# Kernel optimization log

Measured on AMD Instinct MI355X. Metric: run time of the kernel, lower is better.

## Reference

```python
import jax, jax.numpy as jnp
import numpy as np

EPS = 1e-8


def _laplace_normalize(edge_row, edge_col, edge_vals, num_nodes):
    # D_r^{-1/2} A D_c^{-1/2} as in laplace_transform
    deg_r = jax.ops.segment_sum(edge_vals, edge_row, num_segments=num_nodes)
    deg_c = jax.ops.segment_sum(edge_vals, edge_col, num_segments=num_nodes)
    inv_r = 1.0 / (jnp.sqrt(deg_r) + EPS)
    inv_c = 1.0 / (jnp.sqrt(deg_c) + EPS)
    return edge_vals * inv_r[edge_row] * inv_c[edge_col]


def _l2norm(x):
    # F.normalize(p=2, dim=1): x / max(||x||, eps) with eps=1e-12
    n = jnp.sqrt(jnp.sum(x * x, axis=1, keepdims=True))
    return x / jnp.maximum(n, 1e-12)


def setup_inputs() -> dict:
    key = jax.random.key(0)
    k1, k2, k3, k4, k5, k6 = jax.random.split(key, 6)
    N, D, E, B = 100000, 64, 3200000, 4096
    node_features = jax.random.normal(k1, (N, D), dtype=jnp.float32)
    edge_row = jax.random.randint(k2, (E,), 0, N, dtype=jnp.int32)
    edge_col = jax.random.randint(k3, (E,), 0, N, dtype=jnp.int32)
    edge_vals = jnp.ones((E,), dtype=jnp.float32)
    a_id = jax.random.randint(k4, (B,), 0, N, dtype=jnp.int32)
    pos_id = jax.random.randint(k5, (B,), 0, N, dtype=jnp.int32)
    neg_id = jax.random.randint(k6, (B,), 0, N, dtype=jnp.int32)
    return {"node_features": node_features, "edge_row": edge_row,
            "edge_col": edge_col, "edge_vals": edge_vals,
            "a_id": a_id, "pos_id": pos_id, "neg_id": neg_id}


def reference(node_features, edge_row, edge_col, edge_vals, a_id, pos_id, neg_id):
    num_nodes = node_features.shape[0]
    num_layers = 3
    norm_vals = _laplace_normalize(edge_row, edge_col, edge_vals, num_nodes)

    # one_propagate: repeated spmm + per-layer L2 normalize, mean over layers
    features = node_features
    acc = node_features  # layer-0 term of the running sum (not normalized)
    for _ in range(num_layers):
        msgs = norm_vals[:, None] * features[edge_col]  # [E, D]
        features = jax.ops.segment_sum(msgs, edge_row, num_segments=num_nodes)
        acc = acc + _l2norm(features)
    node_rep = acc / (num_layers + 1)

    # BPR loss over batch
    a = node_rep[a_id]
    pos_pred = jnp.sum(a * node_rep[pos_id], axis=1)
    neg_pred = jnp.sum(a * node_rep[neg_id], axis=1)
    loss = jnp.mean(-jax.nn.log_sigmoid(pos_pred - neg_pred))
    return loss
```

## Files before the change

kernel.cpp:

```cpp
#include <hip/hip_runtime.h>
#include <math.h>

#define DDIM 64
#define BUCKET 1024
#define LRSHIFT 17
#define CMASK 0x1FFFF
#define LRMASK 0x3FF
#define NBLK 512
#define TPB_BIN 1024
#define NWV 16
#define MAXNB 128

typedef unsigned long long ull;
typedef _Float16 half2_t __attribute__((ext_vector_type(2)));

__device__ inline unsigned int bf16_hi(float v) {
    unsigned int a = __float_as_uint(v);
    return (a + 0x7fffu + ((a >> 16) & 1u)) & 0xffff0000u;
}

__device__ inline unsigned int pk_f16x2(float lo, float hi) {
    return __builtin_bit_cast(unsigned int, __builtin_amdgcn_cvt_pkrtz(lo, hi));
}

__device__ inline half2_t dup_lo16(unsigned int s) {
    return __builtin_bit_cast(half2_t, __builtin_amdgcn_perm(0u, s, 0x01000100u));
}

__device__ inline half2_t h2_shfl_xor(half2_t v, int off) {
    return __builtin_bit_cast(half2_t, __shfl_xor(__builtin_bit_cast(unsigned int, v), off));
}

__global__ void init_fill_kernel(int* __restrict__ gfill_r, int* __restrict__ gfill_c,
                                 int NB, int cap) {
    int k = blockIdx.x * blockDim.x + threadIdx.x;
    if (k < NB) {
        gfill_r[k * 16] = k * cap;
        gfill_c[k * 16] = k * cap;
    }
}

__global__ __launch_bounds__(TPB_BIN)
void binning_kernel(const int* __restrict__ erow, const int* __restrict__ ecol,
                    const float* __restrict__ evals,
                    int* __restrict__ gfill_r, int* __restrict__ gfill_c,
                    ull* __restrict__ br, unsigned int* __restrict__ bc,
                    int E, int NB, int chunk) {
    __shared__ int hr[NWV][MAXNB];
    __shared__ int hc[NWV][MAXNB];
    __shared__ int fr[MAXNB];
    __shared__ int fc[MAXNB];
    int t = threadIdx.x;
    int wv = t >> 6;
    for (int k = t; k < NWV * MAXNB; k += TPB_BIN) { (&hr[0][0])[k] = 0; (&hc[0][0])[k] = 0; }
    __syncthreads();
    int lo = blockIdx.x * chunk;
    int hi = min(E, lo + chunk);
    int nq = (hi - lo) >> 2;
    int rem = (hi - lo) & 3;
    int p0 = t, p1 = t + TPB_BIN;
    bool h0 = p0 < nq, h1 = p1 < nq;
    int4 r40, c40, r41, c41;
    float4 v40, v41;
    if (h0) {
        int i = lo + 4 * p0;
        r40 = *(const int4*)(erow + i);
        c40 = *(const int4*)(ecol + i);
        v40 = *(const float4*)(evals + i);
        atomicAdd(&hr[wv][r40.x >> 10], 1);
        atomicAdd(&hr[wv][r40.y >> 10], 1);
        atomicAdd(&hr[wv][r40.z >> 10], 1);
        atomicAdd(&hr[wv][r40.w >> 10], 1);
        atomicAdd(&hc[wv][c40.x >> 10], 1);
        atomicAdd(&hc[wv][c40.y >> 10], 1);
        atomicAdd(&hc[wv][c40.z >> 10], 1);
        atomicAdd(&hc[wv][c40.w >> 10], 1);
    }
    if (h1) {
        int i = lo + 4 * p1;
        r41 = *(const int4*)(erow + i);
        c41 = *(const int4*)(ecol + i);
        v41 = *(const float4*)(evals + i);
        atomicAdd(&hr[wv][r41.x >> 10], 1);
        atomicAdd(&hr[wv][r41.y >> 10], 1);
        atomicAdd(&hr[wv][r41.z >> 10], 1);
        atomicAdd(&hr[wv][r41.w >> 10], 1);
        atomicAdd(&hc[wv][c41.x >> 10], 1);
        atomicAdd(&hc[wv][c41.y >> 10], 1);
        atomicAdd(&hc[wv][c41.z >> 10], 1);
        atomicAdd(&hc[wv][c41.w >> 10], 1);
    }
    if (t == 0) {
        for (int i = hi - rem; i < hi; i++) {
            atomicAdd(&hr[0][erow[i] >> 10], 1);
            atomicAdd(&hc[0][ecol[i] >> 10], 1);
        }
    }
    __syncthreads();
    if (t < NB) {
        int sr = 0, sc = 0;
        #pragma unroll
        for (int w2 = 0; w2 < NWV; w2++) { sr += hr[w2][t]; sc += hc[w2][t]; }
        fr[t] = atomicAdd(&gfill_r[t * 16], sr);
        fc[t] = atomicAdd(&gfill_c[t * 16], sc);
    }
    __syncthreads();
    if (h0) {
        int pos0 = atomicAdd(&fr[r40.x >> 10], 1);
        int pos1 = atomicAdd(&fr[r40.y >> 10], 1);
        int pos2 = atomicAdd(&fr[r40.z >> 10], 1);
        int pos3 = atomicAdd(&fr[r40.w >> 10], 1);
        br[pos0] = ((ull)__float_as_uint(v40.x) << 32) | ((ull)(r40.x & 1023) << LRSHIFT) | (unsigned)c40.x;
        br[pos1] = ((ull)__float_as_uint(v40.y) << 32) | ((ull)(r40.y & 1023) << LRSHIFT) | (unsigned)c40.y;
        br[pos2] = ((ull)__float_as_uint(v40.z) << 32) | ((ull)(r40.z & 1023) << LRSHIFT) | (unsigned)c40.z;
        br[pos3] = ((ull)__float_as_uint(v40.w) << 32) | ((ull)(r40.w & 1023) << LRSHIFT) | (unsigned)c40.w;
        int q0 = atomicAdd(&fc[c40.x >> 10], 1);
        int q1 = atomicAdd(&fc[c40.y >> 10], 1);
        int q2 = atomicAdd(&fc[c40.z >> 10], 1);
        int q3 = atomicAdd(&fc[c40.w >> 10], 1);
        bc[q0] = bf16_hi(v40.x) | (unsigned)(c40.x & 1023);
        bc[q1] = bf16_hi(v40.y) | (unsigned)(c40.y & 1023);
        bc[q2] = bf16_hi(v40.z) | (unsigned)(c40.z & 1023);
        bc[q3] = bf16_hi(v40.w) | (unsigned)(c40.w & 1023);
    }
    if (h1) {
        int pos0 = atomicAdd(&fr[r41.x >> 10], 1);
        int pos1 = atomicAdd(&fr[r41.y >> 10], 1);
        int pos2 = atomicAdd(&fr[r41.z >> 10], 1);
        int pos3 = atomicAdd(&fr[r41.w >> 10], 1);
        br[pos0] = ((ull)__float_as_uint(v41.x) << 32) | ((ull)(r41.x & 1023) << LRSHIFT) | (unsigned)c41.x;
        br[pos1] = ((ull)__float_as_uint(v41.y) << 32) | ((ull)(r41.y & 1023) << LRSHIFT) | (unsigned)c41.y;
        br[pos2] = ((ull)__float_as_uint(v41.z) << 32) | ((ull)(r41.z & 1023) << LRSHIFT) | (unsigned)c41.z;
        br[pos3] = ((ull)__float_as_uint(v41.w) << 32) | ((ull)(r41.w & 1023) << LRSHIFT) | (unsigned)c41.w;
        int q0 = atomicAdd(&fc[c41.x >> 10], 1);
        int q1 = atomicAdd(&fc[c41.y >> 10], 1);
        int q2 = atomicAdd(&fc[c41.z >> 10], 1);
        int q3 = atomicAdd(&fc[c41.w >> 10], 1);
        bc[q0] = bf16_hi(v41.x) | (unsigned)(c41.x & 1023);
        bc[q1] = bf16_hi(v41.y) | (unsigned)(c41.y & 1023);
        bc[q2] = bf16_hi(v41.z) | (unsigned)(c41.z & 1023);
        bc[q3] = bf16_hi(v41.w) | (unsigned)(c41.w & 1023);
    }
    if (t == 0) {
        for (int i = hi - rem; i < hi; i++) {
            int r = erow[i], c = ecol[i];
            float v = evals[i];
            int pos = atomicAdd(&fr[r >> 10], 1);
            br[pos] = ((ull)__float_as_uint(v) << 32) | ((ull)(r & 1023) << LRSHIFT) | (unsigned)c;
            int pos2 = atomicAdd(&fc[c >> 10], 1);
            bc[pos2] = bf16_hi(v) | (unsigned)(c & 1023);
        }
    }
}

__global__ __launch_bounds__(BUCKET)
void fused_cp_kernel(const ull* __restrict__ br, const unsigned int* __restrict__ bc,
                     const int* __restrict__ gfill_r, const int* __restrict__ gfill_c,
                     int2* __restrict__ rse, float* __restrict__ inv_c,
                     unsigned int* __restrict__ cw, int N, int cap) {
    __shared__ int   cnt[BUCKET];
    __shared__ float ds[BUCKET];
    __shared__ float dsc[BUCKET];
    __shared__ int   sc[BUCKET];
    __shared__ float invr[BUCKET];
    int b = blockIdx.x, t = threadIdx.x;
    cnt[t] = 0; ds[t] = 0.0f; dsc[t] = 0.0f;
    __syncthreads();
    int s = b * cap;
    int e = gfill_r[b * 16];
    int m = s + ((e - s) & ~3);
    for (int i = s + 4 * t; i < m; i += 4 * BUCKET) {
        ull p0 = br[i];
        ull p1 = br[i + 1];
        ull p2 = br[i + 2];
        ull p3 = br[i + 3];
        int lr0 = (int)((p0 >> LRSHIFT) & LRMASK);
        int lr1 = (int)((p1 >> LRSHIFT) & LRMASK);
        int lr2 = (int)((p2 >> LRSHIFT) & LRMASK);
        int lr3 = (int)((p3 >> LRSHIFT) & LRMASK);
        atomicAdd(&cnt[lr0], 1);
        atomicAdd(&cnt[lr1], 1);
        atomicAdd(&cnt[lr2], 1);
        atomicAdd(&cnt[lr3], 1);
        atomicAdd(&ds[lr0], __uint_as_float((unsigned)(p0 >> 32)));
        atomicAdd(&ds[lr1], __uint_as_float((unsigned)(p1 >> 32)));
        atomicAdd(&ds[lr2], __uint_as_float((unsigned)(p2 >> 32)));
        atomicAdd(&ds[lr3], __uint_as_float((unsigned)(p3 >> 32)));
    }
    if (t == 0) {
        for (int i = m; i < e; i++) {
            ull p = br[i];
            int lr = (int)((p >> LRSHIFT) & LRMASK);
            atomicAdd(&cnt[lr], 1);
            atomicAdd(&ds[lr], __uint_as_float((unsigned)(p >> 32)));
        }
    }
    int e2 = gfill_c[b * 16];
    int m2 = s + ((e2 - s) & ~3);
    for (int i = s + 4 * t; i < m2; i += 4 * BUCKET) {
        uint4 p = *(const uint4*)(bc + i);
        atomicAdd(&dsc[p.x & 0x3FFu], __uint_as_float(p.x & 0xffff0000u));
        atomicAdd(&dsc[p.y & 0x3FFu], __uint_as_float(p.y & 0xffff0000u));
        atomicAdd(&dsc[p.z & 0x3FFu], __uint_as_float(p.z & 0xffff0000u));
        atomicAdd(&dsc[p.w & 0x3FFu], __uint_as_float(p.w & 0xffff0000u));
    }
    if (t == 0) {
        for (int i = m2; i < e2; i++) {
            unsigned int p = bc[i];
            atomicAdd(&dsc[p & 0x3FFu], __uint_as_float(p & 0xffff0000u));
        }
    }
    __syncthreads();
    int c0 = cnt[t];
    int sum4 = (c0 + 3) & ~3;
    sc[t] = sum4;
    __syncthreads();
    for (int off = 1; off < BUCKET; off <<= 1) {
        int v = (t >= off) ? sc[t - off] : 0;
        __syncthreads();
        sc[t] += v;
        __syncthreads();
    }
    int st = s + sc[t] - sum4;
    int node = b * BUCKET + t;
    if (node < N) {
        int2 se;
        se.x = st;
        se.y = st + c0;
        rse[node] = se;
    }
    inv_c[node] = 1.0f / (sqrtf(dsc[t]) + 1e-8f);
    invr[t] = 1.0f / (sqrtf(ds[t]) + 1e-8f);
    __syncthreads();
    cnt[t] = st;
    __syncthreads();
    for (int i = s + 4 * t; i < m; i += 4 * BUCKET) {
        ull p0 = br[i];
        ull p1 = br[i + 1];
        ull p2 = br[i + 2];
        ull p3 = br[i + 3];
        int c0_ = (int)(p0 & CMASK), c1_ = (int)(p1 & CMASK);
        int c2_ = (int)(p2 & CMASK), c3_ = (int)(p3 & CMASK);
        int lr0 = (int)((p0 >> LRSHIFT) & LRMASK);
        int lr1 = (int)((p1 >> LRSHIFT) & LRMASK);
        int lr2 = (int)((p2 >> LRSHIFT) & LRMASK);
        int lr3 = (int)((p3 >> LRSHIFT) & LRMASK);
        float v0 = __uint_as_float((unsigned)(p0 >> 32));
        float v1 = __uint_as_float((unsigned)(p1 >> 32));
        float v2 = __uint_as_float((unsigned)(p2 >> 32));
        float v3 = __uint_as_float((unsigned)(p3 >> 32));
        int pos0 = atomicAdd(&cnt[lr0], 1);
        int pos1 = atomicAdd(&cnt[lr1], 1);
        int pos2 = atomicAdd(&cnt[lr2], 1);
        int pos3 = atomicAdd(&cnt[lr3], 1);
        float w0 = v0 * invr[lr0];
        float w1 = v1 * invr[lr1];
        float w2 = v2 * invr[lr2];
        float w3 = v3 * invr[lr3];
        cw[pos0] = ((unsigned)c0_ << 15) | ((pk_f16x2(w0, w0) & 0xFFFFu) >> 1);
        cw[pos1] = ((unsigned)c1_ << 15) | ((pk_f16x2(w1, w1) & 0xFFFFu) >> 1);
        cw[pos2] = ((unsigned)c2_ << 15) | ((pk_f16x2(w2, w2) & 0xFFFFu) >> 1);
        cw[pos3] = ((unsigned)c3_ << 15) | ((pk_f16x2(w3, w3) & 0xFFFFu) >> 1);
    }
    if (t == 0) {
        for (int i = m; i < e; i++) {
            ull p = br[i];
            int c = (int)(p & CMASK);
            int lr = (int)((p >> LRSHIFT) & LRMASK);
            float v = __uint_as_float((unsigned)(p >> 32));
            int pos = atomicAdd(&cnt[lr], 1);
            float wv = v * invr[lr];
            cw[pos] = ((unsigned)c << 15) | ((pk_f16x2(wv, wv) & 0xFFFFu) >> 1);
        }
    }
}

__global__ void cvt_kernel(const float* __restrict__ src, const float* __restrict__ inv_c,
                           unsigned int* __restrict__ dst, long n4) {
    long i = (long)blockIdx.x * blockDim.x + threadIdx.x;
    if (i < n4) {
        float ic = inv_c[i >> 4];
        float4 v = ((const float4*)src)[i];
        uint2 o;
        o.x = pk_f16x2(v.x * ic, v.y * ic);
        o.y = pk_f16x2(v.z * ic, v.w * ic);
        ((uint2*)dst)[i] = o;
    }
}

__global__ __launch_bounds__(256)
void spmm_f16_kernel(const int2* __restrict__ rse,
                     const unsigned int* __restrict__ cw,
                     const float* __restrict__ inv_c,
                     const unsigned short* __restrict__ fin,
                     unsigned short* __restrict__ fout, int N) {
    int wid = blockIdx.x * (blockDim.x >> 6) + (threadIdx.x >> 6);
    if (wid >= N) return;
    int lane = threadIdx.x & 63;
    int g = lane >> 3;
    int h = lane & 7;
    int2 se = rse[wid];
    float ic = inv_c[wid];
    int s = se.x, e = se.y;
    half2_t a2[8];
    #pragma unroll
    for (int k = 0; k < 8; k++) a2[k] = (half2_t)0;

    for (int base = s; base < e; base += 32) {
        int j = base + 4 * g;
        if (j < e) {
            uint4 pw = *(const uint4*)(cw + j);
            int c0 = (int)(pw.x >> 15);
            int c1 = (j + 1 < e) ? (int)(pw.y >> 15) : c0;
            int c2 = (j + 2 < e) ? (int)(pw.z >> 15) : c0;
            int c3 = (j + 3 < e) ? (int)(pw.w >> 15) : c0;
            uint4 q0 = ((const uint4*)(fin + ((long)c0 << 6)))[h];
            uint4 q1 = ((const uint4*)(fin + ((long)c1 << 6)))[h];
            uint4 q2 = ((const uint4*)(fin + ((long)c2 << 6)))[h];
            uint4 q3 = ((const uint4*)(fin + ((long)c3 << 6)))[h];
            half2_t w0 = dup_lo16(pw.x << 1);
            half2_t w1 = (j + 1 < e) ? dup_lo16(pw.y << 1) : (half2_t)0;
            half2_t w2 = (j + 2 < e) ? dup_lo16(pw.z << 1) : (half2_t)0;
            half2_t w3 = (j + 3 < e) ? dup_lo16(pw.w << 1) : (half2_t)0;
            a2[0] += w0 * __builtin_bit_cast(half2_t, q0.x);
            a2[1] += w0 * __builtin_bit_cast(half2_t, q0.y);
            a2[2] += w0 * __builtin_bit_cast(half2_t, q0.z);
            a2[3] += w0 * __builtin_bit_cast(half2_t, q0.w);
            a2[4] += w1 * __builtin_bit_cast(half2_t, q1.x);
            a2[5] += w1 * __builtin_bit_cast(half2_t, q1.y);
            a2[6] += w1 * __builtin_bit_cast(half2_t, q1.z);
            a2[7] += w1 * __builtin_bit_cast(half2_t, q1.w);
            a2[0] += w2 * __builtin_bit_cast(half2_t, q2.x);
            a2[1] += w2 * __builtin_bit_cast(half2_t, q2.y);
            a2[2] += w2 * __builtin_bit_cast(half2_t, q2.z);
            a2[3] += w2 * __builtin_bit_cast(half2_t, q2.w);
            a2[4] += w3 * __builtin_bit_cast(half2_t, q3.x);
            a2[5] += w3 * __builtin_bit_cast(half2_t, q3.y);
            a2[6] += w3 * __builtin_bit_cast(half2_t, q3.z);
            a2[7] += w3 * __builtin_bit_cast(half2_t, q3.w);
        }
    }

    #pragma unroll
    for (int k = 0; k < 4; k++) a2[k] += a2[k + 4];
    #pragma unroll
    for (int k = 0; k < 4; k++) {
        a2[k] += h2_shfl_xor(a2[k], 8);
        a2[k] += h2_shfl_xor(a2[k], 16);
        a2[k] += h2_shfl_xor(a2[k], 32);
    }
    if (g == 0) {
        half2_t ich = __builtin_bit_cast(half2_t, pk_f16x2(ic, ic));
        uint4 o;
        o.x = __builtin_bit_cast(unsigned int, a2[0] * ich);
        o.y = __builtin_bit_cast(unsigned int, a2[1] * ich);
        o.z = __builtin_bit_cast(unsigned int, a2[2] * ich);
        o.w = __builtin_bit_cast(unsigned int, a2[3] * ich);
        ((uint4*)(fout + ((long)wid << 6)))[h] = o;
    }
}

__device__ inline float rep_at(const float* __restrict__ nf,
                               const unsigned short* __restrict__ f1,
                               const unsigned short* __restrict__ f2,
                               const unsigned short* __restrict__ f3,
                               int id, int lane) {
    long off = (long)id * DDIM + lane;
    float r  = nf[off];
    float v1 = (float)__builtin_bit_cast(_Float16, f1[off]);
    float v2 = (float)__builtin_bit_cast(_Float16, f2[off]);
    float v3 = (float)__builtin_bit_cast(_Float16, f3[off]);
    float s1 = v1 * v1, s2 = v2 * v2, s3 = v3 * v3;
    #pragma unroll
    for (int o = 1; o < 64; o <<= 1) {
        s1 += __shfl_xor(s1, o);
        s2 += __shfl_xor(s2, o);
        s3 += __shfl_xor(s3, o);
    }
    r += v1 / fmaxf(sqrtf(s1), 1e-12f);
    r += v2 / fmaxf(sqrtf(s2), 1e-12f);
    r += v3 / fmaxf(sqrtf(s3), 1e-12f);
    return r;
}

__global__ void loss_terms_kernel(const float* __restrict__ nf,
                                  const unsigned short* __restrict__ f1,
                                  const unsigned short* __restrict__ f2,
                                  const unsigned short* __restrict__ f3,
                                  const int* __restrict__ a_id, const int* __restrict__ p_id,
                                  const int* __restrict__ n_id,
                                  float* __restrict__ terms, int B) {
    long gid = (long)blockIdx.x * blockDim.x + threadIdx.x;
    int b = (int)(gid >> 6);
    int lane = threadIdx.x & 63;
    if (b < B) {
        float ra = rep_at(nf, f1, f2, f3, a_id[b], lane);
        float rp = rep_at(nf, f1, f2, f3, p_id[b], lane);
        float rn = rep_at(nf, f1, f2, f3, n_id[b], lane);
        float dp = ra * rp, dn = ra * rn;
        #pragma unroll
        for (int off = 1; off < 64; off <<= 1) { dp += __shfl_xor(dp, off); dn += __shfl_xor(dn, off); }
        if (lane == 0) {
            float x = (dp - dn) * 0.0625f;
            terms[b] = fmaxf(-x, 0.0f) + log1pf(expf(-fabsf(x)));
        }
    }
}

__global__ void reduce_kernel(const float* __restrict__ terms, float* __restrict__ out, int B) {
    __shared__ float sm[256];
    float s = 0.0f;
    for (int i = threadIdx.x; i < B; i += 256) s += terms[i];
    sm[threadIdx.x] = s;
    __syncthreads();
    for (int stride = 128; stride > 0; stride >>= 1) {
        if (threadIdx.x < stride) sm[threadIdx.x] += sm[threadIdx.x + stride];
        __syncthreads();
    }
    if (threadIdx.x == 0) out[0] = sm[0] / (float)B;
}

extern "C" void kernel_launch(void* const* d_in, const int* in_sizes, int n_in,
                              void* d_out, int out_size, void* d_ws, size_t ws_size,
                              hipStream_t stream) {
    const float* nf    = (const float*)d_in[0];
    const int*   erow  = (const int*)d_in[1];
    const int*   ecol  = (const int*)d_in[2];
    const float* evals = (const float*)d_in[3];
    const int*   a_id  = (const int*)d_in[4];
    const int*   p_id  = (const int*)d_in[5];
    const int*   n_id  = (const int*)d_in[6];

    int N = in_sizes[0] / DDIM;
    int E = in_sizes[1];
    int B = in_sizes[4];
    int NB = (N + BUCKET - 1) / BUCKET;
    int chunk = (((E + NBLK - 1) / NBLK) + 3) & ~3;
    int Npad = NB * BUCKET;

    long capl = ((long)E * BUCKET) / N;
    int cap = (int)(capl + capl / 12 + 5120);
    cap = (cap + 63) & ~63;

    size_t regionA = (size_t)cap * NB * 8;
    size_t regionB = (size_t)cap * NB * 4;
    size_t featB16 = (size_t)N * DDIM * 2;
    if (regionA < 2 * featB16) regionA = 2 * featB16;

    char* w = (char*)d_ws;
    ull*  br     = (ull*)w;
    char* regAp  = w;                 w += regionA;
    unsigned int* bc = (unsigned int*)w;
    unsigned int* cw = (unsigned int*)w;  w += regionB + 256;
    unsigned short* fb2 = (unsigned short*)w;  w += featB16;
    float* inv_c = (float*)w;         w += (size_t)Npad * 4;
    int2* rse    = (int2*)w;          w += (size_t)N * 8;
    int* gfill_r = (int*)w;           w += (size_t)NB * 16 * 4;
    int* gfill_c = (int*)w;           w += (size_t)NB * 16 * 4;
    float* terms = (float*)w;         w += (size_t)B * 4;

    unsigned short* fb0 = (unsigned short*)regAp;
    unsigned short* fb1 = (unsigned short*)(regAp + featB16);

    init_fill_kernel<<<1, 128, 0, stream>>>(gfill_r, gfill_c, NB, cap);
    binning_kernel<<<NBLK, TPB_BIN, 0, stream>>>(erow, ecol, evals, gfill_r, gfill_c,
                                                 br, bc, E, NB, chunk);
    fused_cp_kernel<<<NB, BUCKET, 0, stream>>>(br, bc, gfill_r, gfill_c,
                                               rse, inv_c, cw, N, cap);

    long n4 = (long)N * DDIM / 4;
    cvt_kernel<<<(unsigned)((n4 + 255) / 256), 256, 0, stream>>>(nf, inv_c, (unsigned int*)fb0, n4);

    unsigned spmmGrid = (unsigned)((N + 3) / 4);
    spmm_f16_kernel<<<spmmGrid, 256, 0, stream>>>(rse, cw, inv_c, fb0, fb1, N);
    spmm_f16_kernel<<<spmmGrid, 256, 0, stream>>>(rse, cw, inv_c, fb1, fb2, N);
    spmm_f16_kernel<<<spmmGrid, 256, 0, stream>>>(rse, cw, inv_c, fb2, fb0, N);

    loss_terms_kernel<<<(unsigned)(((long)B * 64 + 255) / 256), 256, 0, stream>>>(
        nf, fb1, fb2, fb0, a_id, p_id, n_id, terms, B);
    reduce_kernel<<<1, 256, 0, stream>>>(terms, (float*)d_out, B);
}
```

Baseline: 410.8 us.

## Split fused degree/CSR build kernel into four sub-blocks per row bucket

The fused kernel that computes degrees and builds the compressed-row layout now launches four blocks per 1024-node bucket instead of one. Every block still recomputes the full bucket's row counts and prefix scan. Each block then handles only its 256-node quarter for the degree sums, the inverse norms and the scatter of packed column/weight entries. The aim is to fill more compute units, since there are only about a hundred buckets. The cost is reading each bucket's edge data four times and repeating the count and scan work.

After: 358.3 us. -12.8%, faster.

```diff
diff --git a/kernel.cpp b/kernel.cpp
--- a/kernel.cpp
+++ b/kernel.cpp
@@ -3,6 +3,7 @@
 
 #define DDIM 64
 #define BUCKET 1024
+#define SUBB 256
 #define LRSHIFT 17
 #define CMASK 0x1FFFF
 #define LRMASK 0x3FF
@@ -153,18 +154,21 @@
     }
 }
 
-__global__ __launch_bounds__(BUCKET)
+__global__ __launch_bounds__(1024)
 void fused_cp_kernel(const ull* __restrict__ br, const unsigned int* __restrict__ bc,
                      const int* __restrict__ gfill_r, const int* __restrict__ gfill_c,
                      int2* __restrict__ rse, float* __restrict__ inv_c,
                      unsigned int* __restrict__ cw, int N, int cap) {
     __shared__ int   cnt[BUCKET];
-    __shared__ float ds[BUCKET];
-    __shared__ float dsc[BUCKET];
     __shared__ int   sc[BUCKET];
-    __shared__ float invr[BUCKET];
-    int b = blockIdx.x, t = threadIdx.x;
-    cnt[t] = 0; ds[t] = 0.0f; dsc[t] = 0.0f;
+    __shared__ float ds[SUBB];
+    __shared__ float dsc[SUBB];
+    __shared__ float invr[SUBB];
+    __shared__ int   cur[SUBB];
+    int b = blockIdx.x >> 2, q = blockIdx.x & 3;
+    int t = threadIdx.x;
+    cnt[t] = 0;
+    if (t < SUBB) { ds[t] = 0.0f; dsc[t] = 0.0f; }
     __syncthreads();
     int s = b * cap;
     int e = gfill_r[b * 16];
@@ -182,37 +186,42 @@
         atomicAdd(&cnt[lr1], 1);
         atomicAdd(&cnt[lr2], 1);
         atomicAdd(&cnt[lr3], 1);
-        atomicAdd(&ds[lr0], __uint_as_float((unsigned)(p0 >> 32)));
-        atomicAdd(&ds[lr1], __uint_as_float((unsigned)(p1 >> 32)));
-        atomicAdd(&ds[lr2], __uint_as_float((unsigned)(p2 >> 32)));
-        atomicAdd(&ds[lr3], __uint_as_float((unsigned)(p3 >> 32)));
+        if ((lr0 >> 8) == q) atomicAdd(&ds[lr0 & 255], __uint_as_float((unsigned)(p0 >> 32)));
+        if ((lr1 >> 8) == q) atomicAdd(&ds[lr1 & 255], __uint_as_float((unsigned)(p1 >> 32)));
+        if ((lr2 >> 8) == q) atomicAdd(&ds[lr2 & 255], __uint_as_float((unsigned)(p2 >> 32)));
+        if ((lr3 >> 8) == q) atomicAdd(&ds[lr3 & 255], __uint_as_float((unsigned)(p3 >> 32)));
     }
     if (t == 0) {
         for (int i = m; i < e; i++) {
             ull p = br[i];
             int lr = (int)((p >> LRSHIFT) & LRMASK);
             atomicAdd(&cnt[lr], 1);
-            atomicAdd(&ds[lr], __uint_as_float((unsigned)(p >> 32)));
+            if ((lr >> 8) == q) atomicAdd(&ds[lr & 255], __uint_as_float((unsigned)(p >> 32)));
         }
     }
     int e2 = gfill_c[b * 16];
     int m2 = s + ((e2 - s) & ~3);
     for (int i = s + 4 * t; i < m2; i += 4 * BUCKET) {
         uint4 p = *(const uint4*)(bc + i);
-        atomicAdd(&dsc[p.x & 0x3FFu], __uint_as_float(p.x & 0xffff0000u));
-        atomicAdd(&dsc[p.y & 0x3FFu], __uint_as_float(p.y & 0xffff0000u));
-        atomicAdd(&dsc[p.z & 0x3FFu], __uint_as_float(p.z & 0xffff0000u));
-        atomicAdd(&dsc[p.w & 0x3FFu], __uint_as_float(p.w & 0xffff0000u));
+        int lc0 = (int)(p.x & 0x3FFu);
+        int lc1 = (int)(p.y & 0x3FFu);
+        int lc2 = (int)(p.z & 0x3FFu);
+        int lc3 = (int)(p.w & 0x3FFu);
+        if ((lc0 >> 8) == q) atomicAdd(&dsc[lc0 & 255], __uint_as_float(p.x & 0xffff0000u));
+        if ((lc1 >> 8) == q) atomicAdd(&dsc[lc1 & 255], __uint_as_float(p.y & 0xffff0000u));
+        if ((lc2 >> 8) == q) atomicAdd(&dsc[lc2 & 255], __uint_as_float(p.z & 0xffff0000u));
+        if ((lc3 >> 8) == q) atomicAdd(&dsc[lc3 & 255], __uint_as_float(p.w & 0xffff0000u));
     }
     if (t == 0) {
         for (int i = m2; i < e2; i++) {
             unsigned int p = bc[i];
-            atomicAdd(&dsc[p & 0x3FFu], __uint_as_float(p & 0xffff0000u));
-        }
-    }
-    __syncthreads();
-    int c0 = cnt[t];
-    int sum4 = (c0 + 3) & ~3;
+            int lc = (int)(p & 0x3FFu);
+            if ((lc >> 8) == q) atomicAdd(&dsc[lc & 255], __uint_as_float(p & 0xffff0000u));
+        }
+    }
+    __syncthreads();
+    int c0v = cnt[t];
+    int sum4 = (c0v + 3) & ~3;
     sc[t] = sum4;
     __syncthreads();
     for (int off = 1; off < BUCKET; off <<= 1) {
@@ -222,55 +231,58 @@
         __syncthreads();
     }
     int st = s + sc[t] - sum4;
-    int node = b * BUCKET + t;
-    if (node < N) {
-        int2 se;
-        se.x = st;
-        se.y = st + c0;
-        rse[node] = se;
-    }
-    inv_c[node] = 1.0f / (sqrtf(dsc[t]) + 1e-8f);
-    invr[t] = 1.0f / (sqrtf(ds[t]) + 1e-8f);
-    __syncthreads();
-    cnt[t] = st;
+    if ((t >> 8) == q) {
+        int node = b * BUCKET + t;
+        if (node < N) {
+            int2 se;
+            se.x = st;
+            se.y = st + c0v;
+            rse[node] = se;
+        }
+        inv_c[node] = 1.0f / (sqrtf(dsc[t & 255]) + 1e-8f);
+        invr[t & 255] = 1.0f / (sqrtf(ds[t & 255]) + 1e-8f);
+        cur[t & 255] = st;
+    }
     __syncthreads();
     for (int i = s + 4 * t; i < m; i += 4 * BUCKET) {
         ull p0 = br[i];
         ull p1 = br[i + 1];
         ull p2 = br[i + 2];
         ull p3 = br[i + 3];
-        int c0_ = (int)(p0 & CMASK), c1_ = (int)(p1 & CMASK);
-        int c2_ = (int)(p2 & CMASK), c3_ = (int)(p3 & CMASK);
         int lr0 = (int)((p0 >> LRSHIFT) & LRMASK);
         int lr1 = (int)((p1 >> LRSHIFT) & LRMASK);
         int lr2 = (int)((p2 >> LRSHIFT) & LRMASK);
         int lr3 = (int)((p3 >> LRSHIFT) & LRMASK);
-        float v0 = __uint_as_float((unsigned)(p0 >> 32));
-        float v1 = __uint_as_float((unsigned)(p1 >> 32));
-        float v2 = __uint_as_float((unsigned)(p2 >> 32));
-        float v3 = __uint_as_float((unsigned)(p3 >> 32));
-        int pos0 = atomicAdd(&cnt[lr0], 1);
-        int pos1 = atomicAdd(&cnt[lr1], 1);
-        int pos2 = atomicAdd(&cnt[lr2], 1);
-        int pos3 = atomicAdd(&cnt[lr3], 1);
-        float w0 = v0 * invr[lr0];
-        float w1 = v1 * invr[lr1];
-        float w2 = v2 * invr[lr2];
-        float w3 = v3 * invr[lr3];
-        cw[pos0] = ((unsigned)c0_ << 15) | ((pk_f16x2(w0, w0) & 0xFFFFu) >> 1);
-        cw[pos1] = ((unsigned)c1_ << 15) | ((pk_f16x2(w1, w1) & 0xFFFFu) >> 1);
-        cw[pos2] = ((unsigned)c2_ << 15) | ((pk_f16x2(w2, w2) & 0xFFFFu) >> 1);
-        cw[pos3] = ((unsigned)c3_ << 15) | ((pk_f16x2(w3, w3) & 0xFFFFu) >> 1);
+        if ((lr0 >> 8) == q) {
+            int pos = atomicAdd(&cur[lr0 & 255], 1);
+            float wv = __uint_as_float((unsigned)(p0 >> 32)) * invr[lr0 & 255];
+            cw[pos] = ((unsigned)(p0 & CMASK) << 15) | ((pk_f16x2(wv, wv) & 0xFFFFu) >> 1);
+        }
+        if ((lr1 >> 8) == q) {
+            int pos = atomicAdd(&cur[lr1 & 255], 1);
+            float wv = __uint_as_float((unsigned)(p1 >> 32)) * invr[lr1 & 255];
+            cw[pos] = ((unsigned)(p1 & CMASK) << 15) | ((pk_f16x2(wv, wv) & 0xFFFFu) >> 1);
+        }
+        if ((lr2 >> 8) == q) {
+            int pos = atomicAdd(&cur[lr2 & 255], 1);
+            float wv = __uint_as_float((unsigned)(p2 >> 32)) * invr[lr2 & 255];
+            cw[pos] = ((unsigned)(p2 & CMASK) << 15) | ((pk_f16x2(wv, wv) & 0xFFFFu) >> 1);
+        }
+        if ((lr3 >> 8) == q) {
+            int pos = atomicAdd(&cur[lr3 & 255], 1);
+            float wv = __uint_as_float((unsigned)(p3 >> 32)) * invr[lr3 & 255];
+            cw[pos] = ((unsigned)(p3 & CMASK) << 15) | ((pk_f16x2(wv, wv) & 0xFFFFu) >> 1);
+        }
     }
     if (t == 0) {
         for (int i = m; i < e; i++) {
             ull p = br[i];
-            int c = (int)(p & CMASK);
             int lr = (int)((p >> LRSHIFT) & LRMASK);
-            float v = __uint_as_float((unsigned)(p >> 32));
-            int pos = atomicAdd(&cnt[lr], 1);
-            float wv = v * invr[lr];
-            cw[pos] = ((unsigned)c << 15) | ((pk_f16x2(wv, wv) & 0xFFFFu) >> 1);
+            if ((lr >> 8) == q) {
+                int pos = atomicAdd(&cur[lr & 255], 1);
+                float wv = __uint_as_float((unsigned)(p >> 32)) * invr[lr & 255];
+                cw[pos] = ((unsigned)(p & CMASK) << 15) | ((pk_f16x2(wv, wv) & 0xFFFFu) >> 1);
+            }
         }
     }
 }
@@ -465,8 +477,8 @@
     init_fill_kernel<<<1, 128, 0, stream>>>(gfill_r, gfill_c, NB, cap);
     binning_kernel<<<NBLK, TPB_BIN, 0, stream>>>(erow, ecol, evals, gfill_r, gfill_c,
                                                  br, bc, E, NB, chunk);
-    fused_cp_kernel<<<NB, BUCKET, 0, stream>>>(br, bc, gfill_r, gfill_c,
-                                               rse, inv_c, cw, N, cap);
+    fused_cp_kernel<<<NB * 4, BUCKET, 0, stream>>>(br, bc, gfill_r, gfill_c,
+                                                   rse, inv_c, cw, N, cap);
 
     long n4 = (long)N * DDIM / 4;
     cvt_kernel<<<(unsigned)((n4 + 255) / 256), 256, 0, stream>>>(nf, inv_c, (unsigned int*)fb0, n4);
```

## Split per-bucket count/place across four blocks and fuse feature convert and loss reduce

Applied to the files above, without the earlier changes.

The single per-bucket count-and-place kernel (NB≈98 blocks) is split into a count kernel and a scan+place kernel, each launched with four blocks per bucket. The count kernel writes partial histograms and degree sums to global memory. The place kernel sums these partials, scans them, and computes each quarter's starting offset. The fp16 feature conversion is folded into the place kernel, and the loss reduce is fused into the loss kernel with a global atomicAdd, removing two launches. The aim is to raise GPU occupancy during CSR construction, which previously ran on fewer blocks than the device has CUs; the cost is an extra kernel boundary, partial buffers, and redundant scans in each of the four blocks.

Result: faster. 393.1 us (-4.3%).

```diff
diff --git a/kernel.cpp b/kernel.cpp
--- a/kernel.cpp
+++ b/kernel.cpp
@@ -32,12 +32,13 @@
 }
 
 __global__ void init_fill_kernel(int* __restrict__ gfill_r, int* __restrict__ gfill_c,
-                                 int NB, int cap) {
+                                 float* __restrict__ out, int NB, int cap) {
     int k = blockIdx.x * blockDim.x + threadIdx.x;
     if (k < NB) {
         gfill_r[k * 16] = k * cap;
         gfill_c[k * 16] = k * cap;
     }
+    if (k == 0) out[0] = 0.0f;
 }
 
 __global__ __launch_bounds__(TPB_BIN)
@@ -153,23 +154,24 @@
     }
 }
 
-__global__ __launch_bounds__(BUCKET)
-void fused_cp_kernel(const ull* __restrict__ br, const unsigned int* __restrict__ bc,
-                     const int* __restrict__ gfill_r, const int* __restrict__ gfill_c,
-                     int2* __restrict__ rse, float* __restrict__ inv_c,
-                     unsigned int* __restrict__ cw, int N, int cap) {
+__global__ __launch_bounds__(1024)
+void count_kernel(const ull* __restrict__ br, const unsigned int* __restrict__ bc,
+                  const int* __restrict__ gfill_r, const int* __restrict__ gfill_c,
+                  int* __restrict__ subcnt, float* __restrict__ subds,
+                  float* __restrict__ subdsc, int cap) {
     __shared__ int   cnt[BUCKET];
     __shared__ float ds[BUCKET];
     __shared__ float dsc[BUCKET];
-    __shared__ int   sc[BUCKET];
-    __shared__ float invr[BUCKET];
-    int b = blockIdx.x, t = threadIdx.x;
+    int b = blockIdx.x >> 2, q = blockIdx.x & 3;
+    int t = threadIdx.x;
     cnt[t] = 0; ds[t] = 0.0f; dsc[t] = 0.0f;
     __syncthreads();
     int s = b * cap;
     int e = gfill_r[b * 16];
-    int m = s + ((e - s) & ~3);
-    for (int i = s + 4 * t; i < m; i += 4 * BUCKET) {
+    int ql = ((((e - s) + 3) >> 2) + 3) & ~3;
+    int cs = s + q * ql, ce = min(e, cs + ql); if (ce < cs) ce = cs;
+    int m = cs + ((ce - cs) & ~3);
+    for (int i = cs + 4 * t; i < m; i += 4 * 1024) {
         ull p0 = br[i];
         ull p1 = br[i + 1];
         ull p2 = br[i + 2];
@@ -188,7 +190,7 @@
         atomicAdd(&ds[lr3], __uint_as_float((unsigned)(p3 >> 32)));
     }
     if (t == 0) {
-        for (int i = m; i < e; i++) {
+        for (int i = m; i < ce; i++) {
             ull p = br[i];
             int lr = (int)((p >> LRSHIFT) & LRMASK);
             atomicAdd(&cnt[lr], 1);
@@ -196,8 +198,10 @@
         }
     }
     int e2 = gfill_c[b * 16];
-    int m2 = s + ((e2 - s) & ~3);
-    for (int i = s + 4 * t; i < m2; i += 4 * BUCKET) {
+    int ql2 = ((((e2 - s) + 3) >> 2) + 3) & ~3;
+    int cs2 = s + q * ql2, ce2 = min(e2, cs2 + ql2); if (ce2 < cs2) ce2 = cs2;
+    int m2 = cs2 + ((ce2 - cs2) & ~3);
+    for (int i = cs2 + 4 * t; i < m2; i += 4 * 1024) {
         uint4 p = *(const uint4*)(bc + i);
         atomicAdd(&dsc[p.x & 0x3FFu], __uint_as_float(p.x & 0xffff0000u));
         atomicAdd(&dsc[p.y & 0x3FFu], __uint_as_float(p.y & 0xffff0000u));
@@ -205,14 +209,42 @@
         atomicAdd(&dsc[p.w & 0x3FFu], __uint_as_float(p.w & 0xffff0000u));
     }
     if (t == 0) {
-        for (int i = m2; i < e2; i++) {
+        for (int i = m2; i < ce2; i++) {
             unsigned int p = bc[i];
             atomicAdd(&dsc[p & 0x3FFu], __uint_as_float(p & 0xffff0000u));
         }
     }
     __syncthreads();
-    int c0 = cnt[t];
-    int sum4 = (c0 + 3) & ~3;
+    size_t base = ((size_t)(b * 4 + q)) * BUCKET;
+    subcnt[base + t] = cnt[t];
+    subds[base + t]  = ds[t];
+    subdsc[base + t] = dsc[t];
+}
+
+__global__ __launch_bounds__(1024)
+void scanplace_kernel(const ull* __restrict__ br, const int* __restrict__ gfill_r,
+                      const int* __restrict__ subcnt, const float* __restrict__ subds,
+                      const float* __restrict__ subdsc,
+                      const float* __restrict__ nf, unsigned short* __restrict__ fb0,
+                      int2* __restrict__ rse, float* __restrict__ inv_c,
+                      unsigned int* __restrict__ cw, int N, int cap) {
+    __shared__ int   sc[BUCKET];
+    __shared__ int   cur[BUCKET];
+    __shared__ float invr[BUCKET];
+    __shared__ float invc_sh[256];
+    int b = blockIdx.x >> 2, q = blockIdx.x & 3;
+    int t = threadIdx.x;
+    size_t base = (size_t)b * 4 * BUCKET;
+    int c0 = subcnt[base + t];
+    int c1 = subcnt[base + BUCKET + t];
+    int c2 = subcnt[base + 2 * BUCKET + t];
+    int c3 = subcnt[base + 3 * BUCKET + t];
+    float dsum = subds[base + t] + subds[base + BUCKET + t]
+               + subds[base + 2 * BUCKET + t] + subds[base + 3 * BUCKET + t];
+    float dcsum = subdsc[base + t] + subdsc[base + BUCKET + t]
+                + subdsc[base + 2 * BUCKET + t] + subdsc[base + 3 * BUCKET + t];
+    int total = c0 + c1 + c2 + c3;
+    int sum4 = (total + 3) & ~3;
     sc[t] = sum4;
     __syncthreads();
     for (int off = 1; off < BUCKET; off <<= 1) {
@@ -221,70 +253,72 @@
         sc[t] += v;
         __syncthreads();
     }
+    int s = b * cap;
     int st = s + sc[t] - sum4;
+    int offq = (q > 0 ? c0 : 0) + (q > 1 ? c1 : 0) + (q > 2 ? c2 : 0);
+    cur[t] = st + offq;
+    invr[t] = 1.0f / (sqrtf(dsum) + 1e-8f);
+    float icv = 1.0f / (sqrtf(dcsum) + 1e-8f);
     int node = b * BUCKET + t;
-    if (node < N) {
-        int2 se;
-        se.x = st;
-        se.y = st + c0;
-        rse[node] = se;
-    }
-    inv_c[node] = 1.0f / (sqrtf(dsc[t]) + 1e-8f);
-    invr[t] = 1.0f / (sqrtf(ds[t]) + 1e-8f);
-    __syncthreads();
-    cnt[t] = st;
-    __syncthreads();
-    for (int i = s + 4 * t; i < m; i += 4 * BUCKET) {
+    if ((t >> 8) == q) {
+        if (node < N) {
+            int2 se;
+            se.x = st;
+            se.y = st + total;
+            rse[node] = se;
+            inv_c[node] = icv;
+        }
+        invc_sh[t & 255] = icv;
+    }
+    __syncthreads();
+    int e = gfill_r[b * 16];
+    int ql = ((((e - s) + 3) >> 2) + 3) & ~3;
+    int cs = s + q * ql, ce = min(e, cs + ql); if (ce < cs) ce = cs;
+    int m = cs + ((ce - cs) & ~3);
+    for (int i = cs + 4 * t; i < m; i += 4 * 1024) {
         ull p0 = br[i];
         ull p1 = br[i + 1];
         ull p2 = br[i + 2];
         ull p3 = br[i + 3];
-        int c0_ = (int)(p0 & CMASK), c1_ = (int)(p1 & CMASK);
-        int c2_ = (int)(p2 & CMASK), c3_ = (int)(p3 & CMASK);
         int lr0 = (int)((p0 >> LRSHIFT) & LRMASK);
         int lr1 = (int)((p1 >> LRSHIFT) & LRMASK);
         int lr2 = (int)((p2 >> LRSHIFT) & LRMASK);
         int lr3 = (int)((p3 >> LRSHIFT) & LRMASK);
-        float v0 = __uint_as_float((unsigned)(p0 >> 32));
-        float v1 = __uint_as_float((unsigned)(p1 >> 32));
-        float v2 = __uint_as_float((unsigned)(p2 >> 32));
-        float v3 = __uint_as_float((unsigned)(p3 >> 32));
-        int pos0 = atomicAdd(&cnt[lr0], 1);
-        int pos1 = atomicAdd(&cnt[lr1], 1);
-        int pos2 = atomicAdd(&cnt[lr2], 1);
-        int pos3 = atomicAdd(&cnt[lr3], 1);
-        float w0 = v0 * invr[lr0];
-        float w1 = v1 * invr[lr1];
-        float w2 = v2 * invr[lr2];
-        float w3 = v3 * invr[lr3];
-        cw[pos0] = ((unsigned)c0_ << 15) | ((pk_f16x2(w0, w0) & 0xFFFFu) >> 1);
-        cw[pos1] = ((unsigned)c1_ << 15) | ((pk_f16x2(w1, w1) & 0xFFFFu) >> 1);
-        cw[pos2] = ((unsigned)c2_ << 15) | ((pk_f16x2(w2, w2) & 0xFFFFu) >> 1);
-        cw[pos3] = ((unsigned)c3_ << 15) | ((pk_f16x2(w3, w3) & 0xFFFFu) >> 1);
+        int pos0 = atomicAdd(&cur[lr0], 1);
+        int pos1 = atomicAdd(&cur[lr1], 1);
+        int pos2 = atomicAdd(&cur[lr2], 1);
+        int pos3 = atomicAdd(&cur[lr3], 1);
+        float w0 = __uint_as_float((unsigned)(p0 >> 32)) * invr[lr0];
+        float w1 = __uint_as_float((unsigned)(p1 >> 32)) * invr[lr1];
+        float w2 = __uint_as_float((unsigned)(p2 >> 32)) * invr[lr2];
+        float w3 = __uint_as_float((unsigned)(p3 >> 32)) * invr[lr3];
+        cw[pos0] = ((unsigned)(p0 & CMASK) << 15) | ((pk_f16x2(w0, w0) & 0xFFFFu) >> 1);
+        cw[pos1] = ((unsigned)(p1 & CMASK) << 15) | ((pk_f16x2(w1, w1) & 0xFFFFu) >> 1);
+        cw[pos2] = ((unsigned)(p2 & CMASK) << 15) | ((pk_f16x2(w2, w2) & 0xFFFFu) >> 1);
+        cw[pos3] = ((unsigned)(p3 & CMASK) << 15) | ((pk_f16x2(w3, w3) & 0xFFFFu) >> 1);
     }
     if (t == 0) {
-        for (int i = m; i < e; i++) {
+        for (int i = m; i < ce; i++) {
             ull p = br[i];
-            int c = (int)(p & CMASK);
             int lr = (int)((p >> LRSHIFT) & LRMASK);
-            float v = __uint_as_float((unsigned)(p >> 32));
-            int pos = atomicAdd(&cnt[lr], 1);
-            float wv = v * invr[lr];
-            cw[pos] = ((unsigned)c << 15) | ((pk_f16x2(wv, wv) & 0xFFFFu) >> 1);
-        }
-    }
-}
-
-__global__ void cvt_kernel(const float* __restrict__ src, const float* __restrict__ inv_c,
-                           unsigned int* __restrict__ dst, long n4) {
-    long i = (long)blockIdx.x * blockDim.x + threadIdx.x;
-    if (i < n4) {
-        float ic = inv_c[i >> 4];
-        float4 v = ((const float4*)src)[i];
-        uint2 o;
-        o.x = pk_f16x2(v.x * ic, v.y * ic);
-        o.y = pk_f16x2(v.z * ic, v.w * ic);
-        ((uint2*)dst)[i] = o;
+            int pos = atomicAdd(&cur[lr], 1);
+            float wv = __uint_as_float((unsigned)(p >> 32)) * invr[lr];
+            cw[pos] = ((unsigned)(p & CMASK) << 15) | ((pk_f16x2(wv, wv) & 0xFFFFu) >> 1);
+        }
+    }
+    int n0 = b * BUCKET + (q << 8);
+    const float4* nf4 = (const float4*)nf;
+    uint2* fb0u = (uint2*)fb0;
+    for (int k = t; k < 4096; k += 1024) {
+        int nodek = n0 + (k >> 4);
+        if (nodek < N) {
+            float4 v = nf4[(long)n0 * 16 + k];
+            float ic = invc_sh[k >> 4];
+            uint2 o;
+            o.x = pk_f16x2(v.x * ic, v.y * ic);
+            o.y = pk_f16x2(v.z * ic, v.w * ic);
+            fb0u[(long)n0 * 16 + k] = o;
+        }
     }
 }
 
@@ -383,16 +417,19 @@
     return r;
 }
 
-__global__ void loss_terms_kernel(const float* __restrict__ nf,
-                                  const unsigned short* __restrict__ f1,
-                                  const unsigned short* __restrict__ f2,
-                                  const unsigned short* __restrict__ f3,
-                                  const int* __restrict__ a_id, const int* __restrict__ p_id,
-                                  const int* __restrict__ n_id,
-                                  float* __restrict__ terms, int B) {
+__global__ void loss_kernel(const float* __restrict__ nf,
+                            const unsigned short* __restrict__ f1,
+                            const unsigned short* __restrict__ f2,
+                            const unsigned short* __restrict__ f3,
+                            const int* __restrict__ a_id, const int* __restrict__ p_id,
+                            const int* __restrict__ n_id,
+                            float* __restrict__ out, int B, float invB) {
+    __shared__ float sm[4];
     long gid = (long)blockIdx.x * blockDim.x + threadIdx.x;
     int b = (int)(gid >> 6);
     int lane = threadIdx.x & 63;
+    int wv = threadIdx.x >> 6;
+    float term = 0.0f;
     if (b < B) {
         float ra = rep_at(nf, f1, f2, f3, a_id[b], lane);
         float rp = rep_at(nf, f1, f2, f3, p_id[b], lane);
@@ -400,24 +437,14 @@
         float dp = ra * rp, dn = ra * rn;
         #pragma unroll
         for (int off = 1; off < 64; off <<= 1) { dp += __shfl_xor(dp, off); dn += __shfl_xor(dn, off); }
-        if (lane == 0) {
-            float x = (dp - dn) * 0.0625f;
-            terms[b] = fmaxf(-x, 0.0f) + log1pf(expf(-fabsf(x)));
-        }
-    }
-}
-
-__global__ void reduce_kernel(const float* __restrict__ terms, float* __restrict__ out, int B) {
-    __shared__ float sm[256];
-    float s = 0.0f;
-    for (int i = threadIdx.x; i < B; i += 256) s += terms[i];
-    sm[threadIdx.x] = s;
-    __syncthreads();
-    for (int stride = 128; stride > 0; stride >>= 1) {
-        if (threadIdx.x < stride) sm[threadIdx.x] += sm[threadIdx.x + stride];
-        __syncthreads();
-    }
-    if (threadIdx.x == 0) out[0] = sm[0] / (float)B;
+        float x = (dp - dn) * 0.0625f;
+        term = fmaxf(-x, 0.0f) + log1pf(expf(-fabsf(x)));
+    }
+    if (lane == 0) sm[wv] = term;
+    __syncthreads();
+    if (threadIdx.x == 0) {
+        atomicAdd(out, (sm[0] + sm[1] + sm[2] + sm[3]) * invB);
+    }
 }
 
 extern "C" void kernel_launch(void* const* d_in, const int* in_sizes, int n_in,
@@ -445,38 +472,39 @@
     size_t regionA = (size_t)cap * NB * 8;
     size_t regionB = (size_t)cap * NB * 4;
     size_t featB16 = (size_t)N * DDIM * 2;
-    if (regionA < 2 * featB16) regionA = 2 * featB16;
+    if (regionA < featB16) regionA = featB16;
+    size_t subBytes = (size_t)NB * 4 * BUCKET * 4;
 
     char* w = (char*)d_ws;
     ull*  br     = (ull*)w;
     char* regAp  = w;                 w += regionA;
     unsigned int* bc = (unsigned int*)w;
     unsigned int* cw = (unsigned int*)w;  w += regionB + 256;
+    unsigned short* fb0 = (unsigned short*)w;  w += featB16;
     unsigned short* fb2 = (unsigned short*)w;  w += featB16;
+    int* subcnt  = (int*)w;           w += subBytes;
+    float* subds = (float*)w;         w += subBytes;
+    float* subdsc= (float*)w;         w += subBytes;
     float* inv_c = (float*)w;         w += (size_t)Npad * 4;
     int2* rse    = (int2*)w;          w += (size_t)N * 8;
     int* gfill_r = (int*)w;           w += (size_t)NB * 16 * 4;
     int* gfill_c = (int*)w;           w += (size_t)NB * 16 * 4;
-    float* terms = (float*)w;         w += (size_t)B * 4;
-
-    unsigned short* fb0 = (unsigned short*)regAp;
-    unsigned short* fb1 = (unsigned short*)(regAp + featB16);
-
-    init_fill_kernel<<<1, 128, 0, stream>>>(gfill_r, gfill_c, NB, cap);
+
+    unsigned short* fb1 = (unsigned short*)regAp;
+
+    init_fill_kernel<<<1, 128, 0, stream>>>(gfill_r, gfill_c, (float*)d_out, NB, cap);
     binning_kernel<<<NBLK, TPB_BIN, 0, stream>>>(erow, ecol, evals, gfill_r, gfill_c,
                                                  br, bc, E, NB, chunk);
-    fused_cp_kernel<<<NB, BUCKET, 0, stream>>>(br, bc, gfill_r, gfill_c,
-                                               rse, inv_c, cw, N, cap);
-
-    long n4 = (long)N * DDIM / 4;
-    cvt_kernel<<<(unsigned)((n4 + 255) / 256), 256, 0, stream>>>(nf, inv_c, (unsigned int*)fb0, n4);
+    count_kernel<<<NB * 4, 1024, 0, stream>>>(br, bc, gfill_r, gfill_c,
+                                              subcnt, subds, subdsc, cap);
+    scanplace_kernel<<<NB * 4, 1024, 0, stream>>>(br, gfill_r, subcnt, subds, subdsc,
+                                                  nf, fb0, rse, inv_c, cw, N, cap);
 
     unsigned spmmGrid = (unsigned)((N + 3) / 4);
     spmm_f16_kernel<<<spmmGrid, 256, 0, stream>>>(rse, cw, inv_c, fb0, fb1, N);
     spmm_f16_kernel<<<spmmGrid, 256, 0, stream>>>(rse, cw, inv_c, fb1, fb2, N);
     spmm_f16_kernel<<<spmmGrid, 256, 0, stream>>>(rse, cw, inv_c, fb2, fb0, N);
 
-    loss_terms_kernel<<<(unsigned)(((long)B * 64 + 255) / 256), 256, 0, stream>>>(
-        nf, fb1, fb2, fb0, a_id, p_id, n_id, terms, B);
-    reduce_kernel<<<1, 256, 0, stream>>>(terms, (float*)d_out, B);
-}
+    loss_kernel<<<(unsigned)(((long)B * 64 + 255) / 256), 256, 0, stream>>>(
+        nf, fb1, fb2, fb0, a_id, p_id, n_id, (float*)d_out, B, 1.0f / (float)B);
+}
```
